# Optimization experiments

Measured on AMD Instinct MI355X. Metric: run time of the kernel, lower is better.

The kernel has to match this reference:

```python
import jax, jax.numpy as jnp
import numpy as np

D_MODEL = 1024
NUM_HEADS = 16
D_K = D_MODEL // NUM_HEADS

def setup_inputs() -> dict:
    key = jax.random.key(0)
    ks = jax.random.split(key, 8)
    B, S, D = 2, 2048, D_MODEL
    scale = 1.0 / np.sqrt(D)
    return {
        "X_q": jax.random.normal(ks[0], (B, S, D), dtype=jnp.float32),
        "X_k": jax.random.normal(ks[1], (B, S, D), dtype=jnp.float32),
        "X_v": jax.random.normal(ks[2], (B, S, D), dtype=jnp.float32),
        "W_q": jax.random.normal(ks[3], (D, D), dtype=jnp.float32) * scale,
        "W_k": jax.random.normal(ks[4], (D, D), dtype=jnp.float32) * scale,
        "W_v": jax.random.normal(ks[5], (D, D), dtype=jnp.float32) * scale,
        "W_o": jax.random.normal(ks[6], (D, D), dtype=jnp.float32) * scale,
        "b_o": jnp.zeros((D,), dtype=jnp.float32),
    }

def reference(X_q, X_k, X_v, W_q, W_k, W_v, W_o, b_o):
    B, S, D = X_q.shape
    H, dk = NUM_HEADS, D_K
    # nn.Linear: x @ W.T
    Q = (X_q @ W_q.T).reshape(B, H, S, dk)  # faithful raw view, no transpose
    K = (X_k @ W_k.T).reshape(B, H, S, dk)
    V = (X_v @ W_v.T).reshape(B, H, S, dk)
    A = jnp.einsum("bhqd,bhkd->bhqk", Q, K) / np.sqrt(dk)  # [B,H,S,S]
    A = jax.nn.softmax(A, axis=-1)
    H_cat = jnp.einsum("bhqk,bhkd->bhqd", A, V).reshape(B, S, D)
    return H_cat @ W_o.T + b_o
```

## Files before the change

### kernel.cpp

```cpp
#include <hip/hip_runtime.h>

typedef __bf16 bf16;
typedef bf16 bf16x8 __attribute__((ext_vector_type(8)));
typedef bf16 bf16x4 __attribute__((ext_vector_type(4)));
typedef bf16 bf16x2 __attribute__((ext_vector_type(2)));
typedef float f32x4 __attribute__((ext_vector_type(4)));
typedef float f32x16 __attribute__((ext_vector_type(16)));
typedef int i32x4 __attribute__((ext_vector_type(4)));

#define XSZ 4194304
#define WSZ 1048576
#define KDIM 1024
#define QSCALE 0.1803368801111137f

__device__ __forceinline__ void async16(const bf16* g, bf16* l) {
  __builtin_amdgcn_global_load_lds(
      (const __attribute__((address_space(1))) unsigned int*)g,
      (__attribute__((address_space(3))) unsigned int*)l, 16, 0, 0);
}

__device__ __forceinline__ bf16x8 ld8(const bf16* p) {
  bf16x4 lo = *(const bf16x4*)p;
  bf16x4 hi = *(const bf16x4*)(p + 4);
  return __builtin_shufflevector(lo, hi, 0, 1, 2, 3, 4, 5, 6, 7);
}

__device__ __forceinline__ void st8s(bf16* p, bf16x8 v) {
  *(bf16x4*)p       = __builtin_shufflevector(v, v, 0, 1, 2, 3);
  *(bf16x4*)(p + 4) = __builtin_shufflevector(v, v, 4, 5, 6, 7);
}

__device__ __forceinline__ f32x4 mfma16(bf16x8 a, bf16x8 b, f32x4 c) {
  return __builtin_amdgcn_mfma_f32_16x16x32_bf16(a, b, c, 0, 0, 0);
}
__device__ __forceinline__ f32x16 mfma32(bf16x8 a, bf16x8 b, f32x16 c) {
  return __builtin_amdgcn_mfma_f32_32x32x16_bf16(a, b, c, 0, 0, 0);
}

__device__ __forceinline__ int packbf2(float lo, float hi) {
  bf16x2 t; t[0] = (bf16)lo; t[1] = (bf16)hi;
  return __builtin_bit_cast(int, t);
}

__device__ __forceinline__ float fast_exp2(float x) {
#if __has_builtin(__builtin_amdgcn_exp2f)
  return __builtin_amdgcn_exp2f(x);
#else
  return exp2f(x);
#endif
}

__global__ __launch_bounds__(256) void cast_all(const float* __restrict__ Xq, const float* __restrict__ Xk,
                                                const float* __restrict__ Xv, const float* __restrict__ Wq,
                                                const float* __restrict__ Wk, const float* __restrict__ Wv,
                                                const float* __restrict__ Wo, bf16* __restrict__ dst) {
  size_t i = ((size_t)blockIdx.x * 256 + threadIdx.x) * 8;
  const float* src; size_t off; float scale = 1.0f;
  if (i < XSZ)                { src = Xq; off = i; }
  else if (i < 2 * (size_t)XSZ) { src = Xk; off = i - XSZ; }
  else if (i < 3 * (size_t)XSZ) { src = Xv; off = i - 2 * (size_t)XSZ; }
  else if (i < 3 * (size_t)XSZ + WSZ) { src = Wq; off = i - 3 * (size_t)XSZ; scale = QSCALE; }
  else if (i < 3 * (size_t)XSZ + 2 * (size_t)WSZ) { src = Wk; off = i - 3 * (size_t)XSZ - WSZ; }
  else if (i < 3 * (size_t)XSZ + 3 * (size_t)WSZ) { src = Wv; off = i - 3 * (size_t)XSZ - 2 * (size_t)WSZ; }
  else                        { src = Wo; off = i - 3 * (size_t)XSZ - 3 * (size_t)WSZ; }
  float4 a = *(const float4*)(src + off);
  float4 b = *(const float4*)(src + off + 4);
  bf16x8 o;
  o[0] = (bf16)(a.x * scale); o[1] = (bf16)(a.y * scale);
  o[2] = (bf16)(a.z * scale); o[3] = (bf16)(a.w * scale);
  o[4] = (bf16)(b.x * scale); o[5] = (bf16)(b.y * scale);
  o[6] = (bf16)(b.z * scale); o[7] = (bf16)(b.w * scale);
  *(bf16x8*)(dst + i) = o;
}

__device__ __forceinline__ void gemm_nt_core(const bf16* __restrict__ A, const bf16* __restrict__ Bm,
                                             int m0, int n0, bf16* lds, f32x4 acc[4][4]) {
  const int t = threadIdx.x;
  const int lane = t & 63, wave = t >> 6;
  const int wm = wave & 1, wn = wave >> 1;
  const int quad = lane >> 4, m16 = lane & 15;
  bf16* As = lds;
  bf16* Bs = lds + 128 * 32;
  const int c0 = t, c1 = t + 256;
  const bf16* ga0 = A + (size_t)(m0 + (c0 >> 2)) * KDIM + (c0 & 3) * 8;
  const bf16* ga1 = A + (size_t)(m0 + (c1 >> 2)) * KDIM + (c1 & 3) * 8;
  const bf16* gb0 = Bm + (size_t)(n0 + (c0 >> 2)) * KDIM + (c0 & 3) * 8;
  const bf16* gb1 = Bm + (size_t)(n0 + (c1 >> 2)) * KDIM + (c1 & 3) * 8;
  for (int kt = 0; kt < KDIM; kt += 32) {
    async16(ga0 + kt, As + c0 * 8);
    async16(ga1 + kt, As + c1 * 8);
    async16(gb0 + kt, Bs + c0 * 8);
    async16(gb1 + kt, Bs + c1 * 8);
    __syncthreads();
    bf16x8 af[4], bfv[4];
    #pragma unroll
    for (int i = 0; i < 4; i++)
      af[i] = *(const bf16x8*)(As + (wm * 64 + i * 16 + m16) * 32 + quad * 8);
    #pragma unroll
    for (int i = 0; i < 4; i++)
      bfv[i] = *(const bf16x8*)(Bs + (wn * 64 + i * 16 + m16) * 32 + quad * 8);
    #pragma unroll
    for (int mi = 0; mi < 4; mi++)
      #pragma unroll
      for (int ni = 0; ni < 4; ni++)
        acc[mi][ni] = mfma16(af[mi], bfv[ni], acc[mi][ni]);
    __syncthreads();
  }
}

__global__ __launch_bounds__(256) void proj_gemm(const bf16* __restrict__ xq, const bf16* __restrict__ xk,
                                                 const bf16* __restrict__ xv, const bf16* __restrict__ wq,
                                                 const bf16* __restrict__ wk, const bf16* __restrict__ wv,
                                                 bf16* __restrict__ Qo, bf16* __restrict__ Ko,
                                                 bf16* __restrict__ Vo) {
  __shared__ bf16 lds[2 * 128 * 32];
  const int z = blockIdx.z;
  const bf16* A = (z == 0) ? xq : (z == 1) ? xk : xv;
  const bf16* W = (z == 0) ? wq : (z == 1) ? wk : wv;
  bf16* C = (z == 0) ? Qo : (z == 1) ? Ko : Vo;
  f32x4 acc[4][4];
  #pragma unroll
  for (int i = 0; i < 4; i++)
    #pragma unroll
    for (int j = 0; j < 4; j++) acc[i][j] = (f32x4){0.f, 0.f, 0.f, 0.f};
  gemm_nt_core(A, W, blockIdx.y * 128, blockIdx.x * 128, lds, acc);
  const int lane = threadIdx.x & 63, wave = threadIdx.x >> 6;
  const int wm = wave & 1, wn = wave >> 1, quad = lane >> 4, m16 = lane & 15;
  const int row0 = blockIdx.y * 128 + wm * 64;
  const int col0 = blockIdx.x * 128 + wn * 64;
  #pragma unroll
  for (int mi = 0; mi < 4; mi++)
    #pragma unroll
    for (int ni = 0; ni < 4; ni++)
      #pragma unroll
      for (int r = 0; r < 4; r++) {
        int row = row0 + mi * 16 + quad * 4 + r;
        int col = col0 + ni * 16 + m16;
        C[(size_t)row * 1024 + col] = (bf16)acc[mi][ni][r];
      }
}

__global__ __launch_bounds__(256) void out_gemm(const bf16* __restrict__ Hm, const bf16* __restrict__ wo,
                                                const float* __restrict__ bias, float* __restrict__ out) {
  __shared__ bf16 lds[128 * 32 + 64 * 32];
  bf16* As = lds;
  bf16* Bs = lds + 128 * 32;
  const int t = threadIdx.x;
  const int lane = t & 63, wave = t >> 6;
  const int wm = wave & 1, wn = wave >> 1;
  const int quad = lane >> 4, m16 = lane & 15;
  const int m0 = blockIdx.y * 128, n0 = blockIdx.x * 64;
  const int c0 = t, c1 = t + 256;
  const bf16* ga0 = Hm + (size_t)(m0 + (c0 >> 2)) * KDIM + (c0 & 3) * 8;
  const bf16* ga1 = Hm + (size_t)(m0 + (c1 >> 2)) * KDIM + (c1 & 3) * 8;
  const bf16* gb0 = wo + (size_t)(n0 + (c0 >> 2)) * KDIM + (c0 & 3) * 8;
  f32x4 acc[4][2];
  #pragma unroll
  for (int i = 0; i < 4; i++)
    #pragma unroll
    for (int j = 0; j < 2; j++) acc[i][j] = (f32x4){0.f, 0.f, 0.f, 0.f};
  for (int kt = 0; kt < KDIM; kt += 32) {
    async16(ga0 + kt, As + c0 * 8);
    async16(ga1 + kt, As + c1 * 8);
    if (c0 < 256) async16(gb0 + kt, Bs + c0 * 8);
    __syncthreads();
    bf16x8 af[4], bfv[2];
    #pragma unroll
    for (int i = 0; i < 4; i++)
      af[i] = *(const bf16x8*)(As + (wm * 64 + i * 16 + m16) * 32 + quad * 8);
    #pragma unroll
    for (int i = 0; i < 2; i++)
      bfv[i] = *(const bf16x8*)(Bs + (wn * 32 + i * 16 + m16) * 32 + quad * 8);
    #pragma unroll
    for (int mi = 0; mi < 4; mi++)
      #pragma unroll
      for (int ni = 0; ni < 2; ni++)
        acc[mi][ni] = mfma16(af[mi], bfv[ni], acc[mi][ni]);
    __syncthreads();
  }
  const int row0 = m0 + wm * 64;
  const int col0 = n0 + wn * 32;
  float bv[2];
  #pragma unroll
  for (int ni = 0; ni < 2; ni++) bv[ni] = bias[col0 + ni * 16 + m16];
  #pragma unroll
  for (int mi = 0; mi < 4; mi++)
    #pragma unroll
    for (int ni = 0; ni < 2; ni++)
      #pragma unroll
      for (int r = 0; r < 4; r++) {
        int row = row0 + mi * 16 + quad * 4 + r;
        int col = col0 + ni * 16 + m16;
        out[(size_t)row * 1024 + col] = acc[mi][ni][r] + bv[ni];
      }
}

__global__ __launch_bounds__(256) void transpose_v(const bf16* __restrict__ V, bf16* __restrict__ Vt) {
  __shared__ bf16 T[64 * 65];
  const int t = threadIdx.x;
  const bf16* src = V + (size_t)blockIdx.y * (2048 * 64) + (size_t)blockIdx.x * 64 * 64;
  bf16* dst = Vt + (size_t)blockIdx.y * (2048 * 64) + (size_t)blockIdx.x * 64;
  #pragma unroll
  for (int j = 0; j < 2; j++) {
    int c = t + j * 256;
    int row = c >> 3, col8 = (c & 7) * 8;
    bf16x8 v = *(const bf16x8*)(src + row * 64 + col8);
    #pragma unroll
    for (int i = 0; i < 8; i++) T[row * 65 + col8 + i] = v[i];
  }
  __syncthreads();
  #pragma unroll
  for (int j = 0; j < 2; j++) {
    int c = t + j * 256;
    int d = c >> 3, k8 = (c & 7) * 8;
    bf16x8 o;
    #pragma unroll
    for (int i = 0; i < 8; i++) o[i] = T[(k8 + i) * 65 + d];
    *(bf16x8*)(dst + (size_t)d * 2048 + k8) = o;
  }
}

#define KS 68
#define VS 132
__global__ __launch_bounds__(256, 3) void attn_kernel(const bf16* __restrict__ Qg,
                                                      const bf16* __restrict__ Kg,
                                                      const bf16* __restrict__ Vtg,
                                                      bf16* __restrict__ Hout) {
  __shared__ bf16 smem[128 * KS + 64 * VS];
  bf16* Ks = smem;
  bf16* Vs = smem + 128 * KS;
  const int t = threadIdx.x;
  const int lane = t & 63, w = t >> 6;
  const int l31 = lane & 31, h = lane >> 5;
  const int L = blockIdx.x + 16 * blockIdx.y;
  const int xcd = L & 7, j5 = L >> 3;
  const int bh = xcd * 4 + (j5 & 3);
  const int qt = j5 >> 2;
  const size_t base = (size_t)bh * (2048 * 64);
  const bf16* Kp = Kg + base;
  const bf16* Vp = Vtg + base;
  const int q = qt * 128 + w * 32 + l31;

  bf16x8 qf[4];
  #pragma unroll
  for (int kc = 0; kc < 4; kc++)
    qf[kc] = *(const bf16x8*)(Qg + base + (size_t)q * 64 + 16 * kc + 8 * h);

  f32x16 oacc[2];
  #pragma unroll
  for (int mt = 0; mt < 2; mt++)
    #pragma unroll
    for (int i = 0; i < 16; i++) oacc[mt][i] = 0.f;
  float lrow = 0.f;

  int krow[4], kcol[4], vrow[4], vcol[4];
  #pragma unroll
  for (int j = 0; j < 4; j++) {
    int c = t + j * 256;
    krow[j] = c >> 3;  kcol[j] = (c & 7) * 8;
    vrow[j] = c >> 4;  vcol[j] = (c & 15) * 8;
  }

  bf16x8 kreg[4], vreg[4];
  #pragma unroll
  for (int j = 0; j < 4; j++) {
    kreg[j] = *(const bf16x8*)(Kp + (size_t)krow[j] * 64 + kcol[j]);
    vreg[j] = *(const bf16x8*)(Vp + (size_t)vrow[j] * 2048 + vcol[j]);
  }

  for (int kt = 0; kt < 16; kt++) {
    #pragma unroll
    for (int j = 0; j < 4; j++) st8s(Ks + krow[j] * KS + kcol[j], kreg[j]);
    #pragma unroll
    for (int j = 0; j < 4; j++) st8s(Vs + vrow[j] * VS + vcol[j], vreg[j]);
    __syncthreads();

    if (kt + 1 < 16) {
      #pragma unroll
      for (int j = 0; j < 4; j++) {
        kreg[j] = *(const bf16x8*)(Kp + (size_t)((kt + 1) * 128 + krow[j]) * 64 + kcol[j]);
        vreg[j] = *(const bf16x8*)(Vp + (size_t)vrow[j] * 2048 + (kt + 1) * 128 + vcol[j]);
      }
    }

    #pragma unroll
    for (int mt = 0; mt < 4; mt++) {
      f32x16 sacc;
      #pragma unroll
      for (int i = 0; i < 16; i++) sacc[i] = 0.f;
      #pragma unroll
      for (int kc = 0; kc < 4; kc++) {
        bf16x8 kf = ld8(Ks + (32 * mt + l31) * KS + 16 * kc + 8 * h);
        sacc = mfma32(kf, qf[kc], sacc);
      }
      int pd[8];
      float sum = 0.f;
      #pragma unroll
      for (int p = 0; p < 8; p++) {
        float p0 = fast_exp2(sacc[2 * p]);
        float p1 = fast_exp2(sacc[2 * p + 1]);
        sum += p0 + p1;
        pd[p] = packbf2(p0, p1);
      }
      lrow += sum;
      #pragma unroll
      for (int c1 = 0; c1 < 2; c1++) {
        const int kc = 2 * mt + c1;
        const int rro = 2 * c1 + h;
        const int rrp = 2 * c1 + 1 - h;
        int s0 = __shfl_xor(pd[2 * rrp], 32, 64);
        int s1 = __shfl_xor(pd[2 * rrp + 1], 32, 64);
        int o0 = pd[2 * rro], o1 = pd[2 * rro + 1];
        i32x4 w4;
        w4.x = h ? s0 : o0;
        w4.y = h ? s1 : o1;
        w4.z = h ? o0 : s0;
        w4.w = h ? o1 : s1;
        bf16x8 pfrag = __builtin_bit_cast(bf16x8, w4);
        #pragma unroll
        for (int mtd = 0; mtd < 2; mtd++) {
          bf16x8 vf = ld8(Vs + (32 * mtd + l31) * VS + 16 * kc + 8 * h);
          oacc[mtd] = mfma32(vf, pfrag, oacc[mtd]);
        }
      }
    }
    __syncthreads();
  }

  lrow += __shfl_xor(lrow, 32, 64);
  float inv = 1.f / lrow;
  float* Tf = (float*)smem + w * 2048;
  #pragma unroll
  for (int mt = 0; mt < 2; mt++)
    #pragma unroll
    for (int r = 0; r < 16; r++) {
      int d = 32 * mt + (r & 3) + 8 * (r >> 2) + 4 * h;
      Tf[d * 32 + l31] = oacc[mt][r] * inv;
    }
  __syncthreads();
  bf16* Hq = Hout + base + (size_t)(qt * 128 + w * 32 + l31) * 64 + 32 * h;
  #pragma unroll
  for (int s = 0; s < 4; s++) {
    bf16x8 o;
    #pragma unroll
    for (int i = 0; i < 8; i++) o[i] = (bf16)Tf[(32 * h + s * 8 + i) * 32 + l31];
    *(bf16x8*)(Hq + s * 8) = o;
  }
}

extern "C" void kernel_launch(void* const* d_in, const int* in_sizes, int n_in,
                              void* d_out, int out_size, void* d_ws, size_t ws_size,
                              hipStream_t stream) {
  const float* Xq = (const float*)d_in[0];
  const float* Xk = (const float*)d_in[1];
  const float* Xv = (const float*)d_in[2];
  const float* Wq = (const float*)d_in[3];
  const float* Wk = (const float*)d_in[4];
  const float* Wv = (const float*)d_in[5];
  const float* Wo = (const float*)d_in[6];
  const float* bo = (const float*)d_in[7];

  bf16* ws = (bf16*)d_ws;
  bf16* xq = ws;
  bf16* xk = ws + XSZ;
  bf16* xv = ws + 2 * (size_t)XSZ;
  bf16* wq = ws + 3 * (size_t)XSZ;
  bf16* wk = wq + WSZ;
  bf16* wv = wk + WSZ;
  bf16* wo = wv + WSZ;
  bf16* q  = wo + WSZ;
  bf16* k  = q + XSZ;
  bf16* v  = k + XSZ;
  bf16* vt = xv;
  bf16* h  = xq;

  cast_all<<<8192, 256, 0, stream>>>(Xq, Xk, Xv, Wq, Wk, Wv, Wo, ws);
  proj_gemm<<<dim3(8, 32, 3), 256, 0, stream>>>(xq, xk, xv, wq, wk, wv, q, k, v);
  transpose_v<<<dim3(32, 32), 256, 0, stream>>>(v, vt);
  attn_kernel<<<dim3(16, 32), 256, 0, stream>>>(q, k, vt, h);
  out_gemm<<<dim3(16, 32), 256, 0, stream>>>(h, wo, bo, (float*)d_out);
}
```

Measured before the change: 255.0 us.

## Split attention key range across two wave groups per block and merge outputs

The attention block grows to 512 threads. Two halves each process 8 of the 16 key tiles in separate LDS buffers, and their partial output accumulators and row sums are combined through shared memory at the end. This is meant to double the number of waves working on each query tile, raising parallelism and latency hiding for a grid of only 512 blocks. It costs double LDS per block, an extra reduction step with a sync, and more register pressure under the new launch bounds.

Measured after the change: 303.7 us. 1.19x slower.

```diff
diff --git a/kernel.cpp b/kernel.cpp
--- a/kernel.cpp
+++ b/kernel.cpp
@@ -49,6 +49,7 @@
   return exp2f(x);
 #endif
 }
+
 
 __global__ __launch_bounds__(256) void cast_all(const float* __restrict__ Xq, const float* __restrict__ Xk,
                                                 const float* __restrict__ Xv, const float* __restrict__ Wq,
@@ -222,16 +223,20 @@
 
 #define KS 68
 #define VS 132
-__global__ __launch_bounds__(256, 3) void attn_kernel(const bf16* __restrict__ Qg,
+#define HALF_LDS (128 * KS + 64 * VS)
+__global__ __launch_bounds__(512, 4) void attn_kernel(const bf16* __restrict__ Qg,
                                                       const bf16* __restrict__ Kg,
                                                       const bf16* __restrict__ Vtg,
                                                       bf16* __restrict__ Hout) {
-  __shared__ bf16 smem[128 * KS + 64 * VS];
-  bf16* Ks = smem;
-  bf16* Vs = smem + 128 * KS;
+  __shared__ bf16 smem[2 * HALF_LDS];
   const int t = threadIdx.x;
-  const int lane = t & 63, w = t >> 6;
+  const int lane = t & 63;
+  const int w = (t >> 6) & 3;
+  const int half = t >> 8;
+  const int tt = t & 255;
   const int l31 = lane & 31, h = lane >> 5;
+  bf16* Ks = smem + half * HALF_LDS;
+  bf16* Vs = Ks + 128 * KS;
   const int L = blockIdx.x + 16 * blockIdx.y;
   const int xcd = L & 7, j5 = L >> 3;
   const int bh = xcd * 4 + (j5 & 3);
@@ -256,30 +261,32 @@
   int krow[4], kcol[4], vrow[4], vcol[4];
   #pragma unroll
   for (int j = 0; j < 4; j++) {
-    int c = t + j * 256;
+    int c = tt + j * 256;
     krow[j] = c >> 3;  kcol[j] = (c & 7) * 8;
     vrow[j] = c >> 4;  vcol[j] = (c & 15) * 8;
   }
 
+  const int tile0 = half * 8;
   bf16x8 kreg[4], vreg[4];
   #pragma unroll
   for (int j = 0; j < 4; j++) {
-    kreg[j] = *(const bf16x8*)(Kp + (size_t)krow[j] * 64 + kcol[j]);
-    vreg[j] = *(const bf16x8*)(Vp + (size_t)vrow[j] * 2048 + vcol[j]);
-  }
-
-  for (int kt = 0; kt < 16; kt++) {
+    kreg[j] = *(const bf16x8*)(Kp + (size_t)(tile0 * 128 + krow[j]) * 64 + kcol[j]);
+    vreg[j] = *(const bf16x8*)(Vp + (size_t)vrow[j] * 2048 + tile0 * 128 + vcol[j]);
+  }
+
+  for (int kt = 0; kt < 8; kt++) {
     #pragma unroll
     for (int j = 0; j < 4; j++) st8s(Ks + krow[j] * KS + kcol[j], kreg[j]);
     #pragma unroll
     for (int j = 0; j < 4; j++) st8s(Vs + vrow[j] * VS + vcol[j], vreg[j]);
     __syncthreads();
 
-    if (kt + 1 < 16) {
+    if (kt + 1 < 8) {
+      const int tg = tile0 + kt + 1;
       #pragma unroll
       for (int j = 0; j < 4; j++) {
-        kreg[j] = *(const bf16x8*)(Kp + (size_t)((kt + 1) * 128 + krow[j]) * 64 + kcol[j]);
-        vreg[j] = *(const bf16x8*)(Vp + (size_t)vrow[j] * 2048 + (kt + 1) * 128 + vcol[j]);
+        kreg[j] = *(const bf16x8*)(Kp + (size_t)(tg * 128 + krow[j]) * 64 + kcol[j]);
+        vreg[j] = *(const bf16x8*)(Vp + (size_t)vrow[j] * 2048 + tg * 128 + vcol[j]);
       }
     }
 
@@ -328,23 +335,39 @@
   }
 
   lrow += __shfl_xor(lrow, 32, 64);
-  float inv = 1.f / lrow;
-  float* Tf = (float*)smem + w * 2048;
-  #pragma unroll
-  for (int mt = 0; mt < 2; mt++)
-    #pragma unroll
-    for (int r = 0; r < 16; r++) {
-      int d = 32 * mt + (r & 3) + 8 * (r >> 2) + 4 * h;
-      Tf[d * 32 + l31] = oacc[mt][r] * inv;
-    }
+  float* Sf = (float*)smem;
+  float* Tf = Sf + w * 2048;
+  float* Lb = Sf + 8192 + w * 32;
+  if (half) {
+    #pragma unroll
+    for (int mt = 0; mt < 2; mt++)
+      #pragma unroll
+      for (int r = 0; r < 16; r++) {
+        int d = 32 * mt + (r & 3) + 8 * (r >> 2) + 4 * h;
+        Tf[d * 32 + l31] = oacc[mt][r];
+      }
+    if (!h) Lb[l31] = lrow;
+  }
+  __syncthreads();
+  if (!half) {
+    float linv = 1.f / (lrow + Lb[l31]);
+    #pragma unroll
+    for (int mt = 0; mt < 2; mt++)
+      #pragma unroll
+      for (int r = 0; r < 16; r++) {
+        int d = 32 * mt + (r & 3) + 8 * (r >> 2) + 4 * h;
+        Tf[d * 32 + l31] = (oacc[mt][r] + Tf[d * 32 + l31]) * linv;
+      }
+  }
   __syncthreads();
   bf16* Hq = Hout + base + (size_t)(qt * 128 + w * 32 + l31) * 64 + 32 * h;
   #pragma unroll
-  for (int s = 0; s < 4; s++) {
+  for (int s = 0; s < 2; s++) {
+    int se = half * 2 + s;
     bf16x8 o;
     #pragma unroll
-    for (int i = 0; i < 8; i++) o[i] = (bf16)Tf[(32 * h + s * 8 + i) * 32 + l31];
-    *(bf16x8*)(Hq + s * 8) = o;
+    for (int i = 0; i < 8; i++) o[i] = (bf16)Tf[(32 * h + se * 8 + i) * 32 + l31];
+    *(bf16x8*)(Hq + se * 8) = o;
   }
 }
 
@@ -377,6 +400,6 @@
   cast_all<<<8192, 256, 0, stream>>>(Xq, Xk, Xv, Wq, Wk, Wv, Wo, ws);
   proj_gemm<<<dim3(8, 32, 3), 256, 0, stream>>>(xq, xk, xv, wq, wk, wv, q, k, v);
   transpose_v<<<dim3(32, 32), 256, 0, stream>>>(v, vt);
-  attn_kernel<<<dim3(16, 32), 256, 0, stream>>>(q, k, vt, h);
+  attn_kernel<<<dim3(16, 32), 512, 0, stream>>>(q, k, vt, h);
   out_gemm<<<dim3(16, 32), 256, 0, stream>>>(h, wo, bo, (float*)d_out);
 }
```
